# Kernel tuning notes

Measured on AMD Instinct MI355X. Metric: run time of the kernel, lower is better.

The kernel has to match this reference:

```python
import jax, jax.numpy as jnp
import numpy as np

B, S, E, H = 2, 2048, 1024, 16
D = E // H


def setup_inputs() -> dict:
    key = jax.random.key(0)
    ks = jax.random.split(key, 7)
    return {
        "query": jax.random.normal(ks[0], (B, S, E), dtype=jnp.float32),
        "key": jax.random.normal(ks[1], (B, S, E), dtype=jnp.float32),
        "value": jax.random.normal(ks[2], (B, S, E), dtype=jnp.float32),
        "Wq": jax.random.normal(ks[3], (E, E), dtype=jnp.float32) * (E ** -0.5),
        "Wk": jax.random.normal(ks[4], (E, E), dtype=jnp.float32) * (E ** -0.5),
        "Wv": jax.random.normal(ks[5], (E, E), dtype=jnp.float32) * (E ** -0.5),
        "Wo": jax.random.normal(ks[6], (E, E), dtype=jnp.float32) * (E ** -0.5),
    }


def reference(query, key, value, Wq, Wk, Wv, Wo):
    emb_dim = query.shape[-1]
    h = H
    d = emb_dim // h
    # QuantLinear with all-None quantizers == plain Linear (no bias):
    # torch Linear computes x @ W.T with W of shape [out, in].
    q = query @ Wq.T   # [b, s, e]
    k = key @ Wk.T
    v = value @ Wv.T
    # b s (h d) -> b h s d
    def split_heads(x):
        b, s, e = x.shape
        return x.reshape(b, s, h, d).transpose(0, 2, 1, 3)
    q = split_heads(q)
    k = split_heads(k)
    v = split_heads(v)
    # NOTE: faithful to source — scale uses full emb_dim, not head_dim.
    scale = emb_dim ** (-0.5)
    scores = jnp.einsum('bhsd,bhtd->bhst', q * scale, k)  # [b,h,s,s]
    weights = jax.nn.softmax(scores, axis=-1)  # QuantIdentity(None) == identity; dropout p=0
    heads = jnp.einsum('bhst,bhtd->bhsd', weights, v)
    # b h s d -> b s (h d)
    b = heads.shape[0]
    out = heads.transpose(0, 2, 1, 3).reshape(b, -1, emb_dim)
    return out @ Wo.T
```

## Files before the change

### kernel.cpp

```cpp
#include <hip/hip_runtime.h>
#include <hip/hip_bf16.h>
#include <stdint.h>

typedef __attribute__((ext_vector_type(8))) short s16x8;
typedef __attribute__((ext_vector_type(4))) float f32x4;
typedef __attribute__((ext_vector_type(16))) float f32x16;

#define QSCALE 0.045084220027780106f

__device__ __forceinline__ unsigned short f2bf(float f) {
    union { float f; uint32_t u; } v; v.f = f;
    uint32_t u = v.u;
    u += 0x7FFFu + ((u >> 16) & 1u);
    return (unsigned short)(u >> 16);
}

__device__ __forceinline__ unsigned int pkbf2(float a, float b) {
    union { __hip_bfloat162 h; unsigned int u; } x;
    x.h = __float22bfloat162_rn(float2{a, b});
    return x.u;
}

#define GLOAD_LDS16(gptr, lptr)                                                         \
    __builtin_amdgcn_global_load_lds(                                                   \
        (const __attribute__((address_space(1))) unsigned int*)(gptr),                  \
        (__attribute__((address_space(3))) unsigned int*)(lptr), 16, 0, 0)

__global__ __launch_bounds__(256)
void cvt_all(const float* __restrict__ q, const float* __restrict__ k,
             const float* __restrict__ v, const float* __restrict__ wq,
             const float* __restrict__ wk, const float* __restrict__ wv,
             const float* __restrict__ wo,
             unsigned short* __restrict__ xq, unsigned short* __restrict__ xk,
             unsigned short* __restrict__ xv, unsigned short* __restrict__ wqb,
             unsigned short* __restrict__ wkb, unsigned short* __restrict__ wvb,
             unsigned short* __restrict__ wob)
{
    int bid = blockIdx.x;
    const float* src; unsigned short* dst; int rel;
    if (bid < 6144) {
        int s = bid >> 11; rel = bid & 2047;
        src = (s == 0) ? q : (s == 1) ? k : v;
        dst = (s == 0) ? xq : (s == 1) ? xk : xv;
    } else {
        int s = (bid - 6144) >> 9; rel = (bid - 6144) & 511;
        src = (s == 0) ? wq : (s == 1) ? wk : (s == 2) ? wv : wo;
        dst = (s == 0) ? wqb : (s == 1) ? wkb : (s == 2) ? wvb : wob;
    }
    size_t i = (size_t)rel * 256 + threadIdx.x;
    const float4* p = (const float4*)src;
    float4 a = p[i * 2];
    float4 b2 = p[i * 2 + 1];
    s16x8 r;
    r[0] = (short)f2bf(a.x);  r[1] = (short)f2bf(a.y);
    r[2] = (short)f2bf(a.z);  r[3] = (short)f2bf(a.w);
    r[4] = (short)f2bf(b2.x); r[5] = (short)f2bf(b2.y);
    r[6] = (short)f2bf(b2.z); r[7] = (short)f2bf(b2.w);
    *(s16x8*)(dst + i * 8) = r;
}

__device__ __forceinline__ void gemm_tile512(const unsigned short* __restrict__ A,
                                             const unsigned short* __restrict__ Bt,
                                             void* __restrict__ C,
                                             int N, int K, int mode, float cscale,
                                             unsigned short* Al, unsigned short* Bl,
                                             unsigned short* Tl)
{
    const int tid  = threadIdx.x;
    const int lane = tid & 63;
    const int w    = tid >> 6;
    const int wr   = w >> 2, wc = w & 3;
    const int l15  = lane & 15, l4 = lane >> 4;

    const int m0 = blockIdx.x * 128;
    const int n0 = blockIdx.y * 128;

    f32x4 acc[4][2];
#pragma unroll
    for (int i = 0; i < 4; ++i)
#pragma unroll
        for (int j = 0; j < 2; ++j) acc[i][j] = (f32x4){0.f, 0.f, 0.f, 0.f};

    const int slin = w * 64 + lane;
    const int srow = slin >> 2;
    const int scol = ((slin & 3) ^ ((srow >> 1) & 3)) * 8;

    int aoff[4], boff[2];
#pragma unroll
    for (int mi = 0; mi < 4; ++mi) {
        int rowa = wr * 64 + mi * 16 + l15;
        aoff[mi] = rowa * 32 + ((l4 ^ ((rowa >> 1) & 3)) * 8);
    }
#pragma unroll
    for (int nf = 0; nf < 2; ++nf) {
        int rowb = wc * 32 + nf * 16 + l15;
        boff[nf] = rowb * 32 + ((l4 ^ ((rowb >> 1) & 3)) * 8);
    }

    for (int k0 = 0; k0 < K; k0 += 32) {
        {
            const unsigned short* gA = A + (size_t)(m0 + srow) * K + k0 + scol;
            GLOAD_LDS16(gA, Al + w * 512);
            const unsigned short* gB = Bt + (size_t)(n0 + srow) * K + k0 + scol;
            GLOAD_LDS16(gB, Bl + w * 512);
        }
        __syncthreads();
        s16x8 af[4], bfr[2];
#pragma unroll
        for (int mi = 0; mi < 4; ++mi) af[mi] = *(const s16x8*)(Al + aoff[mi]);
#pragma unroll
        for (int nf = 0; nf < 2; ++nf) bfr[nf] = *(const s16x8*)(Bl + boff[nf]);
#pragma unroll
        for (int mi = 0; mi < 4; ++mi)
#pragma unroll
            for (int nf = 0; nf < 2; ++nf)
                acc[mi][nf] = __builtin_amdgcn_mfma_f32_16x16x32_bf16(af[mi], bfr[nf], acc[mi][nf], 0, 0, 0);
        __syncthreads();
    }

    if (mode == 2) {
        const int b_  = m0 >> 11;
        const int s0g = m0 & 2047;
#pragma unroll
        for (int c0 = 0; c0 < 128; c0 += 32) {
            if (wc == (c0 >> 5)) {
#pragma unroll
                for (int mi = 0; mi < 4; ++mi)
#pragma unroll
                    for (int nf = 0; nf < 2; ++nf) {
                        uint2 pw;
                        pw.x = pkbf2(acc[mi][nf][0], acc[mi][nf][1]);
                        pw.y = pkbf2(acc[mi][nf][2], acc[mi][nf][3]);
                        int c  = nf * 16 + l15;
                        int s4 = wr * 64 + mi * 16 + l4 * 4;
                        *(uint2*)&Tl[c * 136 + s4] = pw;
                    }
            }
            __syncthreads();
            {
                int d  = tid >> 4;
                int sg = tid & 15;
                s16x8 v = *(const s16x8*)&Tl[d * 136 + sg * 8];
                int colg  = n0 + c0 + d;
                int vtrow = (b_ * 16 + (colg >> 6)) * 64 + (colg & 63);
                *(s16x8*)((unsigned short*)C + (size_t)vtrow * 2048 + s0g + sg * 8) = v;
            }
            __syncthreads();
        }
        return;
    }

#pragma unroll
    for (int mi = 0; mi < 4; ++mi)
#pragma unroll
        for (int nf = 0; nf < 2; ++nf)
#pragma unroll
            for (int r = 0; r < 4; ++r) {
                int row = m0 + wr * 64 + mi * 16 + l4 * 4 + r;
                int col = n0 + wc * 32 + nf * 16 + l15;
                float v = acc[mi][nf][r];
                if (mode == 1) ((float*)C)[(size_t)row * N + col] = v;
                else           ((unsigned short*)C)[(size_t)row * N + col] = f2bf(v * cscale);
            }
}

__global__ __launch_bounds__(512, 6)
void gemm_qkv(const unsigned short* __restrict__ A0, const unsigned short* __restrict__ A1,
              const unsigned short* __restrict__ A2,
              const unsigned short* __restrict__ B0, const unsigned short* __restrict__ B1,
              const unsigned short* __restrict__ B2,
              unsigned short* __restrict__ C0, unsigned short* __restrict__ C1,
              unsigned short* __restrict__ C2)
{
    __shared__ unsigned short Al[128 * 32];
    __shared__ unsigned short Bl[128 * 32];
    __shared__ unsigned short Tl[32 * 136];
    int z = blockIdx.z;
    const unsigned short* A  = (z == 0) ? A0 : (z == 1) ? A1 : A2;
    const unsigned short* Bt = (z == 0) ? B0 : (z == 1) ? B1 : B2;
    unsigned short*       C  = (z == 0) ? C0 : (z == 1) ? C1 : C2;
    float cscale = (z == 0) ? QSCALE : 1.0f;
    int mode = (z == 2) ? 2 : 0;
    gemm_tile512(A, Bt, C, 1024, 1024, mode, cscale, Al, Bl, Tl);
}

__global__ __launch_bounds__(512, 6)
void gemm_out(const unsigned short* __restrict__ A, const unsigned short* __restrict__ Bt,
              float* __restrict__ C)
{
    __shared__ unsigned short Al[128 * 32];
    __shared__ unsigned short Bl[128 * 32];
    gemm_tile512(A, Bt, C, 1024, 1024, 1, 1.0f, Al, Bl, nullptr);
}

__global__ __launch_bounds__(512, 4)
void attn8(const unsigned short* __restrict__ Q,
           const unsigned short* __restrict__ Kp,
           const unsigned short* __restrict__ Vt,
           unsigned short* __restrict__ O)
{
    __shared__ unsigned short Kl[2][2][64 * 64];
    __shared__ unsigned short Vl[2][2][64 * 64];

    const int tid  = threadIdx.x;
    const int lane = tid & 63;
    const int w    = tid >> 6;
    const int half = w >> 2, ws = w & 3;
    const int q31  = lane & 31;
    const int lh   = lane >> 5;
    const int m7q  = q31 & 7;
    const int j2   = ((q31 >> 3) & 3) << 1;

    const int hw  = blockIdx.x;
    const int xcd = hw & 7;
    const int idx = hw >> 3;
    const int bh  = xcd * 4 + (idx >> 4);
    const int qt  = idx & 15;
    const int b = bh >> 4, hd = bh & 15;
    const int colbase = hd * 64;
    const int kvbase = half * 1024;

    const size_t qrow = (size_t)(b * 2048 + qt * 128 + ws * 32 + q31);
    s16x8 qf[4];
#pragma unroll
    for (int dk = 0; dk < 4; ++dk)
        qf[dk] = *(const s16x8*)(Q + qrow * 1024 + colbase + dk * 16 + lh * 8);

    int krow[2], kcol[2];
#pragma unroll
    for (int i = 0; i < 2; ++i) {
        int lin = (i * 4 + ws) * 64 + lane;
        krow[i] = lin >> 3;
        int u   = lin & 7;
        kcol[i] = ((u ^ (krow[i] & 7) ^ (((krow[i] >> 3) & 3) << 1)) * 8);
    }

    f32x16 oa[2] = {};
    float l_run = 0.f;

#define STAGE_KV(buf, kv0)                                                                     \
    {                                                                                          \
        _Pragma("unroll")                                                                      \
        for (int i = 0; i < 2; ++i) {                                                          \
            const unsigned short* gk = Kp + (size_t)(b * 2048 + (kv0) + krow[i]) * 1024        \
                                          + colbase + kcol[i];                                 \
            GLOAD_LDS16(gk, &Kl[half][buf][(i * 4 + ws) * 512]);                               \
            const unsigned short* gv = Vt + ((size_t)bh * 64 + krow[i]) * 2048                 \
                                          + (kv0) + kcol[i];                                   \
            GLOAD_LDS16(gv, &Vl[half][buf][(i * 4 + ws) * 512]);                               \
        }                                                                                      \
    }

    STAGE_KV(0, kvbase);
    __syncthreads();

    for (int kt = 0; kt < 16; ++kt) {
        const int cur = kt & 1;
        if (kt < 15) STAGE_KV(cur ^ 1, kvbase + (kt + 1) * 64);

        f32x16 s0 = {}, s1 = {};
#pragma unroll
        for (int dk = 0; dk < 4; ++dk) {
            const int sl = (((dk * 2 + lh) ^ m7q ^ j2) * 8);
            s16x8 kf0 = *(const s16x8*)(&Kl[half][cur][q31 * 64 + sl]);
            s16x8 kf1 = *(const s16x8*)(&Kl[half][cur][(32 + q31) * 64 + sl]);
            s0 = __builtin_amdgcn_mfma_f32_32x32x16_bf16(kf0, qf[dk], s0, 0, 0, 0);
            s1 = __builtin_amdgcn_mfma_f32_32x32x16_bf16(kf1, qf[dk], s1, 0, 0, 0);
        }

        unsigned int PK[2][8];
        float ps = 0.f;
        {
            float p[16];
#pragma unroll
            for (int i = 0; i < 16; ++i) { p[i] = __builtin_amdgcn_exp2f(s0[i]); ps += p[i]; }
#pragma unroll
            for (int j = 0; j < 8; ++j) PK[0][j] = pkbf2(p[2 * j], p[2 * j + 1]);
#pragma unroll
            for (int i = 0; i < 16; ++i) { p[i] = __builtin_amdgcn_exp2f(s1[i]); ps += p[i]; }
#pragma unroll
            for (int j = 0; j < 8; ++j) PK[1][j] = pkbf2(p[2 * j], p[2 * j + 1]);
        }
        l_run += ps;

#pragma unroll
        for (int t = 0; t < 4; ++t) {
            const int bk = t >> 1, j0 = (t & 1) * 4;
            unsigned int A0 = PK[bk][j0],     C0 = PK[bk][j0 + 2];
            unsigned int A1 = PK[bk][j0 + 1], C1 = PK[bk][j0 + 3];
            unsigned int sA0 = (unsigned int)__shfl_xor((int)A0, 32, 64);
            unsigned int sC0 = (unsigned int)__shfl_xor((int)C0, 32, 64);
            unsigned int sA1 = (unsigned int)__shfl_xor((int)A1, 32, 64);
            unsigned int sC1 = (unsigned int)__shfl_xor((int)C1, 32, 64);
            union { unsigned int u[4]; s16x8 v; } pa;
            pa.u[0] = lh ? sC0 : A0;
            pa.u[1] = lh ? sC1 : A1;
            pa.u[2] = lh ? C0 : sA0;
            pa.u[3] = lh ? C1 : sA1;
            const int slv = (((t * 2 + lh) ^ m7q ^ j2) * 8);
            s16x8 vf0 = *(const s16x8*)(&Vl[half][cur][q31 * 64 + slv]);
            s16x8 vf1 = *(const s16x8*)(&Vl[half][cur][(32 + q31) * 64 + slv]);
            oa[0] = __builtin_amdgcn_mfma_f32_32x32x16_bf16(vf0, pa.v, oa[0], 0, 0, 0);
            oa[1] = __builtin_amdgcn_mfma_f32_32x32x16_bf16(vf1, pa.v, oa[1], 0, 0, 0);
        }
        __syncthreads();
    }

    l_run += __shfl_xor(l_run, 32, 64);

    f32x4* Xch = (f32x4*)&Kl[0][0][0];
    float*  Lx = (float*)&Vl[0][0][0];

    if (half == 1) {
#pragma unroll
        for (int dh = 0; dh < 2; ++dh)
#pragma unroll
            for (int rg = 0; rg < 4; ++rg) {
                f32x4 c = { oa[dh][rg * 4 + 0], oa[dh][rg * 4 + 1],
                            oa[dh][rg * 4 + 2], oa[dh][rg * 4 + 3] };
                Xch[((ws * 8 + dh * 4 + rg) << 6) + lane] = c;
            }
        if (lh == 0) Lx[ws * 32 + q31] = l_run;
    }
    __syncthreads();
    if (half == 0) {
        const float lt  = l_run + Lx[ws * 32 + q31];
        const float inv = 1.0f / lt;
#pragma unroll
        for (int dh = 0; dh < 2; ++dh)
#pragma unroll
            for (int rg = 0; rg < 4; ++rg) {
                f32x4 po = Xch[((ws * 8 + dh * 4 + rg) << 6) + lane];
                const int d0 = dh * 32 + rg * 8 + lh * 4;
                uint2 pw;
                pw.x = pkbf2((oa[dh][rg * 4 + 0] + po[0]) * inv,
                             (oa[dh][rg * 4 + 1] + po[1]) * inv);
                pw.y = pkbf2((oa[dh][rg * 4 + 2] + po[2]) * inv,
                             (oa[dh][rg * 4 + 3] + po[3]) * inv);
                *(uint2*)(O + qrow * 1024 + colbase + d0) = pw;
            }
    }
#undef STAGE_KV
}

extern "C" void kernel_launch(void* const* d_in, const int* in_sizes, int n_in,
                              void* d_out, int out_size, void* d_ws, size_t ws_size,
                              hipStream_t stream)
{
    const float* query = (const float*)d_in[0];
    const float* key   = (const float*)d_in[1];
    const float* value = (const float*)d_in[2];
    const float* Wq    = (const float*)d_in[3];
    const float* Wk    = (const float*)d_in[4];
    const float* Wv    = (const float*)d_in[5];
    const float* Wo    = (const float*)d_in[6];
    float* out = (float*)d_out;

    char* ws = (char*)d_ws;
    const size_t SZX = (size_t)4096 * 1024 * 2;
    const size_t SZW = (size_t)1024 * 1024 * 2;
    unsigned short* Xq  = (unsigned short*)(ws + 0);
    unsigned short* Xk  = (unsigned short*)(ws + SZX);
    unsigned short* Xv  = (unsigned short*)(ws + 2 * SZX);
    unsigned short* Wqb = (unsigned short*)(ws + 3 * SZX);
    unsigned short* Wkb = (unsigned short*)(ws + 3 * SZX + SZW);
    unsigned short* Wvb = (unsigned short*)(ws + 3 * SZX + 2 * SZW);
    unsigned short* Wob = (unsigned short*)(ws + 3 * SZX + 3 * SZW);
    unsigned short* Pq  = (unsigned short*)(ws + 3 * SZX + 4 * SZW);
    unsigned short* Pk  = (unsigned short*)(ws + 4 * SZX + 4 * SZW);
    unsigned short* Vt  = (unsigned short*)(ws + 5 * SZX + 4 * SZW);
    unsigned short* AO  = (unsigned short*)(ws + 6 * SZX + 4 * SZW);

    cvt_all<<<8192, 256, 0, stream>>>(query, key, value, Wq, Wk, Wv, Wo,
                                      Xq, Xk, Xv, Wqb, Wkb, Wvb, Wob);
    gemm_qkv<<<dim3(32, 8, 3), 512, 0, stream>>>(Xq, Xk, Xv, Wqb, Wkb, Wvb, Pq, Pk, Vt);
    attn8<<<512, 512, 0, stream>>>(Pq, Pk, Vt, AO);
    gemm_out<<<dim3(32, 8), 512, 0, stream>>>(AO, Wob, out);
}
```

Measured before the change: 123.7 us.

## Split attention KV across four wave groups and add narrower output GEMM tile

```diff
diff --git a/kernel.cpp b/kernel.cpp
--- a/kernel.cpp
+++ b/kernel.cpp
@@ -184,86 +184,126 @@
     gemm_tile512(A, Bt, C, 1024, 1024, mode, cscale, Al, Bl, Tl);
 }
 
-__global__ __launch_bounds__(512, 6)
-void gemm_out(const unsigned short* __restrict__ A, const unsigned short* __restrict__ Bt,
-              float* __restrict__ C)
+__global__ __launch_bounds__(512, 4)
+void gemm_out64(const unsigned short* __restrict__ A, const unsigned short* __restrict__ Bt,
+                float* __restrict__ C)
 {
     __shared__ unsigned short Al[128 * 32];
-    __shared__ unsigned short Bl[128 * 32];
-    gemm_tile512(A, Bt, C, 1024, 1024, 1, 1.0f, Al, Bl, nullptr);
-}
-
-__global__ __launch_bounds__(512, 4)
-void attn8(const unsigned short* __restrict__ Q,
+    __shared__ unsigned short Bl[64 * 32];
+
+    const int tid  = threadIdx.x;
+    const int lane = tid & 63;
+    const int w    = tid >> 6;
+    const int wr   = w >> 1, wc = w & 1;
+    const int l15  = lane & 15, l4 = lane >> 4;
+
+    const int m0 = blockIdx.x * 128;
+    const int n0 = blockIdx.y * 64;
+    const int N = 1024, K = 1024;
+
+    f32x4 acc[2][2];
+#pragma unroll
+    for (int i = 0; i < 2; ++i)
+#pragma unroll
+        for (int j = 0; j < 2; ++j) acc[i][j] = (f32x4){0.f, 0.f, 0.f, 0.f};
+
+    const int slin = w * 64 + lane;
+    const int srow = slin >> 2;
+    const int scol = ((slin & 3) ^ ((srow >> 1) & 3)) * 8;
+    const int brow = (w < 4) ? (slin >> 2) : 0;
+    const int bcol = ((slin & 3) ^ ((brow >> 1) & 3)) * 8;
+
+    int aoff[2], boff[2];
+#pragma unroll
+    for (int mi = 0; mi < 2; ++mi) {
+        int rowa = wr * 32 + mi * 16 + l15;
+        aoff[mi] = rowa * 32 + ((l4 ^ ((rowa >> 1) & 3)) * 8);
+    }
+#pragma unroll
+    for (int nf = 0; nf < 2; ++nf) {
+        int rowb = wc * 32 + nf * 16 + l15;
+        boff[nf] = rowb * 32 + ((l4 ^ ((rowb >> 1) & 3)) * 8);
+    }
+
+    for (int k0 = 0; k0 < K; k0 += 32) {
+        {
+            const unsigned short* gA = A + (size_t)(m0 + srow) * K + k0 + scol;
+            GLOAD_LDS16(gA, Al + w * 512);
+            if (w < 4) {
+                const unsigned short* gB = Bt + (size_t)(n0 + brow) * K + k0 + bcol;
+                GLOAD_LDS16(gB, Bl + w * 512);
+            }
+        }
+        __syncthreads();
+        s16x8 af[2], bfr[2];
+#pragma unroll
+        for (int mi = 0; mi < 2; ++mi) af[mi] = *(const s16x8*)(Al + aoff[mi]);
+#pragma unroll
+        for (int nf = 0; nf < 2; ++nf) bfr[nf] = *(const s16x8*)(Bl + boff[nf]);
+#pragma unroll
+        for (int mi = 0; mi < 2; ++mi)
+#pragma unroll
+            for (int nf = 0; nf < 2; ++nf)
+                acc[mi][nf] = __builtin_amdgcn_mfma_f32_16x16x32_bf16(af[mi], bfr[nf], acc[mi][nf], 0, 0, 0);
+        __syncthreads();
+    }
+
+#pragma unroll
+    for (int mi = 0; mi < 2; ++mi)
+#pragma unroll
+        for (int nf = 0; nf < 2; ++nf)
+#pragma unroll
+            for (int r = 0; r < 4; ++r) {
+                int row = m0 + wr * 32 + mi * 16 + l4 * 4 + r;
+                int col = n0 + wc * 32 + nf * 16 + l15;
+                C[(size_t)row * N + col] = acc[mi][nf][r];
+            }
+}
+
+__global__ __launch_bounds__(512, 8)
+void attn9(const unsigned short* __restrict__ Q,
            const unsigned short* __restrict__ Kp,
            const unsigned short* __restrict__ Vt,
            unsigned short* __restrict__ O)
 {
-    __shared__ unsigned short Kl[2][2][64 * 64];
-    __shared__ unsigned short Vl[2][2][64 * 64];
+    __shared__ f32x4 Xch[4 * 8 * 64];
+    __shared__ float Lx[4][32];
 
     const int tid  = threadIdx.x;
     const int lane = tid & 63;
     const int w    = tid >> 6;
-    const int half = w >> 2, ws = w & 3;
+    const int quarter = w >> 1, sub = w & 1;
     const int q31  = lane & 31;
     const int lh   = lane >> 5;
-    const int m7q  = q31 & 7;
-    const int j2   = ((q31 >> 3) & 3) << 1;
 
     const int hw  = blockIdx.x;
     const int xcd = hw & 7;
     const int idx = hw >> 3;
-    const int bh  = xcd * 4 + (idx >> 4);
-    const int qt  = idx & 15;
+    const int bh  = xcd * 4 + (idx >> 5);
+    const int qt  = idx & 31;
     const int b = bh >> 4, hd = bh & 15;
     const int colbase = hd * 64;
-    const int kvbase = half * 1024;
-
-    const size_t qrow = (size_t)(b * 2048 + qt * 128 + ws * 32 + q31);
+    const int kvbase = quarter * 512;
+
+    const size_t qrow = (size_t)(b * 2048 + qt * 64 + sub * 32 + q31);
     s16x8 qf[4];
 #pragma unroll
     for (int dk = 0; dk < 4; ++dk)
         qf[dk] = *(const s16x8*)(Q + qrow * 1024 + colbase + dk * 16 + lh * 8);
 
-    int krow[2], kcol[2];
-#pragma unroll
-    for (int i = 0; i < 2; ++i) {
-        int lin = (i * 4 + ws) * 64 + lane;
-        krow[i] = lin >> 3;
-        int u   = lin & 7;
-        kcol[i] = ((u ^ (krow[i] & 7) ^ (((krow[i] >> 3) & 3) << 1)) * 8);
-    }
-
     f32x16 oa[2] = {};
     float l_run = 0.f;
 
-#define STAGE_KV(buf, kv0)                                                                     \
-    {                                                                                          \
-        _Pragma("unroll")                                                                      \
-        for (int i = 0; i < 2; ++i) {                                                          \
-            const unsigned short* gk = Kp + (size_t)(b * 2048 + (kv0) + krow[i]) * 1024        \
-                                          + colbase + kcol[i];                                 \
-            GLOAD_LDS16(gk, &Kl[half][buf][(i * 4 + ws) * 512]);                               \
-            const unsigned short* gv = Vt + ((size_t)bh * 64 + krow[i]) * 2048                 \
-                                          + (kv0) + kcol[i];                                   \
-            GLOAD_LDS16(gv, &Vl[half][buf][(i * 4 + ws) * 512]);                               \
-        }                                                                                      \
-    }
-
-    STAGE_KV(0, kvbase);
-    __syncthreads();
-
-    for (int kt = 0; kt < 16; ++kt) {
-        const int cur = kt & 1;
-        if (kt < 15) STAGE_KV(cur ^ 1, kvbase + (kt + 1) * 64);
+    for (int kt = 0; kt < 8; ++kt) {
+        const int kv0 = kvbase + kt * 64;
+        const unsigned short* Kb = Kp + (size_t)(b * 2048 + kv0 + q31) * 1024 + colbase + lh * 8;
+        const unsigned short* Vb = Vt + ((size_t)bh * 64 + q31) * 2048 + kv0 + lh * 8;
 
         f32x16 s0 = {}, s1 = {};
 #pragma unroll
         for (int dk = 0; dk < 4; ++dk) {
-            const int sl = (((dk * 2 + lh) ^ m7q ^ j2) * 8);
-            s16x8 kf0 = *(const s16x8*)(&Kl[half][cur][q31 * 64 + sl]);
-            s16x8 kf1 = *(const s16x8*)(&Kl[half][cur][(32 + q31) * 64 + sl]);
+            s16x8 kf0 = *(const s16x8*)(Kb + dk * 16);
+            s16x8 kf1 = *(const s16x8*)(Kb + 32 * 1024 + dk * 16);
             s0 = __builtin_amdgcn_mfma_f32_32x32x16_bf16(kf0, qf[dk], s0, 0, 0, 0);
             s1 = __builtin_amdgcn_mfma_f32_32x32x16_bf16(kf1, qf[dk], s1, 0, 0, 0);
         }
@@ -297,40 +337,61 @@
             pa.u[1] = lh ? sC1 : A1;
             pa.u[2] = lh ? C0 : sA0;
             pa.u[3] = lh ? C1 : sA1;
-            const int slv = (((t * 2 + lh) ^ m7q ^ j2) * 8);
-            s16x8 vf0 = *(const s16x8*)(&Vl[half][cur][q31 * 64 + slv]);
-            s16x8 vf1 = *(const s16x8*)(&Vl[half][cur][(32 + q31) * 64 + slv]);
+            s16x8 vf0 = *(const s16x8*)(Vb + t * 16);
+            s16x8 vf1 = *(const s16x8*)(Vb + 32 * 2048 + t * 16);
             oa[0] = __builtin_amdgcn_mfma_f32_32x32x16_bf16(vf0, pa.v, oa[0], 0, 0, 0);
             oa[1] = __builtin_amdgcn_mfma_f32_32x32x16_bf16(vf1, pa.v, oa[1], 0, 0, 0);
         }
-        __syncthreads();
     }
 
     l_run += __shfl_xor(l_run, 32, 64);
 
-    f32x4* Xch = (f32x4*)&Kl[0][0][0];
-    float*  Lx = (float*)&Vl[0][0][0];
-
-    if (half == 1) {
+    if (w >= 4) {
+        int wrel = w - 4;
 #pragma unroll
         for (int dh = 0; dh < 2; ++dh)
 #pragma unroll
             for (int rg = 0; rg < 4; ++rg) {
                 f32x4 c = { oa[dh][rg * 4 + 0], oa[dh][rg * 4 + 1],
                             oa[dh][rg * 4 + 2], oa[dh][rg * 4 + 3] };
-                Xch[((ws * 8 + dh * 4 + rg) << 6) + lane] = c;
-            }
-        if (lh == 0) Lx[ws * 32 + q31] = l_run;
+                Xch[((wrel * 8 + dh * 4 + rg) << 6) + lane] = c;
+            }
+        if (lh == 0) Lx[wrel][q31] = l_run;
     }
     __syncthreads();
-    if (half == 0) {
-        const float lt  = l_run + Lx[ws * 32 + q31];
+    if (w < 4) {
+#pragma unroll
+        for (int dh = 0; dh < 2; ++dh)
+#pragma unroll
+            for (int rg = 0; rg < 4; ++rg) {
+                f32x4 po = Xch[((w * 8 + dh * 4 + rg) << 6) + lane];
+                oa[dh][rg * 4 + 0] += po[0]; oa[dh][rg * 4 + 1] += po[1];
+                oa[dh][rg * 4 + 2] += po[2]; oa[dh][rg * 4 + 3] += po[3];
+            }
+        l_run += Lx[w][q31];
+    }
+    __syncthreads();
+    if (w == 2 || w == 3) {
+        int wrel = w - 2;
+#pragma unroll
+        for (int dh = 0; dh < 2; ++dh)
+#pragma unroll
+            for (int rg = 0; rg < 4; ++rg) {
+                f32x4 c = { oa[dh][rg * 4 + 0], oa[dh][rg * 4 + 1],
+                            oa[dh][rg * 4 + 2], oa[dh][rg * 4 + 3] };
+                Xch[((wrel * 8 + dh * 4 + rg) << 6) + lane] = c;
+            }
+        if (lh == 0) Lx[wrel][q31] = l_run;
+    }
+    __syncthreads();
+    if (w < 2) {
+        const float lt  = l_run + Lx[w][q31];
         const float inv = 1.0f / lt;
 #pragma unroll
         for (int dh = 0; dh < 2; ++dh)
 #pragma unroll
             for (int rg = 0; rg < 4; ++rg) {
-                f32x4 po = Xch[((ws * 8 + dh * 4 + rg) << 6) + lane];
+                f32x4 po = Xch[((w * 8 + dh * 4 + rg) << 6) + lane];
                 const int d0 = dh * 32 + rg * 8 + lh * 4;
                 uint2 pw;
                 pw.x = pkbf2((oa[dh][rg * 4 + 0] + po[0]) * inv,
@@ -340,7 +401,6 @@
                 *(uint2*)(O + qrow * 1024 + colbase + d0) = pw;
             }
     }
-#undef STAGE_KV
 }
 
 extern "C" void kernel_launch(void* const* d_in, const int* in_sizes, int n_in,
@@ -374,6 +434,6 @@
     cvt_all<<<8192, 256, 0, stream>>>(query, key, value, Wq, Wk, Wv, Wo,
                                       Xq, Xk, Xv, Wqb, Wkb, Wvb, Wob);
     gemm_qkv<<<dim3(32, 8, 3), 512, 0, stream>>>(Xq, Xk, Xv, Wqb, Wkb, Wvb, Pq, Pk, Vt);
-    attn8<<<512, 512, 0, stream>>>(Pq, Pk, Vt, AO);
-    gemm_out<<<dim3(32, 8), 512, 0, stream>>>(AO, Wob, out);
-}
+    attn9<<<1024, 512, 0, stream>>>(Pq, Pk, Vt, AO);
+    gemm_out64<<<dim3(32, 16), 512, 0, stream>>>(AO, Wob, out);
+}
```

After: 462.8 us. +274.0%, slower.
